# Optimization experiments

Hardware: AMD Instinct MI355X
Metric: run time of the kernel (lower is better)

Reference implementation:

```python
import jax, jax.numpy as jnp
import numpy as np

B, T, C, H = 2, 4096, 1024, 16
HD = C // H  # head dim = 64


def setup_inputs() -> dict:
    key = jax.random.key(0)
    ks = jax.random.split(key, 5)
    s = 1.0 / np.sqrt(C)
    return {
        "x": jax.random.normal(ks[0], (B, T, C), jnp.float32),
        # stored as (in, out) so forward is x @ w + b (equiv to torch Linear with W^T)
        "w_attn": jax.random.normal(ks[1], (C, 3 * C), jnp.float32) * s,
        "b_attn": jax.random.normal(ks[2], (3 * C,), jnp.float32) * 0.02,
        "w_proj": jax.random.normal(ks[3], (C, C), jnp.float32) * s,
        "b_proj": jax.random.normal(ks[4], (C,), jnp.float32) * 0.02,
    }


def reference(x, w_attn, b_attn, w_proj, b_proj):
    # qkv projection: (B,T,3C) -> split into q,k,v
    qkv = x @ w_attn + b_attn
    q, k, v = jnp.split(qkv, 3, axis=-1)
    # (B,T,C) -> (B,H,T,HD)
    def to_heads(t):
        return t.reshape(B, T, H, HD).transpose(0, 2, 1, 3)
    q, k, v = to_heads(q), to_heads(k), to_heads(v)
    # naive attention: explicit (B,H,T,T) scores, causal mask, softmax
    att = jnp.einsum("bhqd,bhkd->bhqk", q, k) * (1.0 / np.sqrt(HD))
    causal = jnp.tril(jnp.ones((T, T), bool))  # (T,T)
    att = jnp.where(causal[None, None], att, -jnp.inf)
    att = jax.nn.softmax(att, axis=-1)
    y = jnp.einsum("bhqk,bhkd->bhqd", att, v)  # (B,H,T,HD)
    y = y.transpose(0, 2, 1, 3).reshape(B, T, C)
    y = y @ w_proj + b_proj
    return (y, (k, v))
```

## Files before the change

kernel.cpp:

```cpp
#include <hip/hip_runtime.h>
#include <hip/hip_bf16.h>

typedef unsigned short u16;
typedef __attribute__((ext_vector_type(8))) short short8;
typedef __attribute__((ext_vector_type(4))) short s16x4;
typedef __attribute__((ext_vector_type(4))) float f32x4;

#define T_SEQ  4096
#define HEADS  16
#define HDIM   64
#define CDIM   1024
#define MDIM   8192
#define HSZ    (T_SEQ * HDIM)
#define SEC    8388608
#define QSCALE 0.1803368801111244f

__device__ __forceinline__ u16 f2bf(float f) {
    __hip_bfloat16 h = __float2bfloat16(f);
    u16 u; __builtin_memcpy(&u, &h, 2);
    return u;
}

__global__ __launch_bounds__(256) void cast_k(const float* __restrict__ in,
                                              u16* __restrict__ out, int n4) {
    const int i = blockIdx.x * 256 + threadIdx.x;
    if (i < n4) {
        f32x4 v = ((const f32x4*)in)[i];
        s16x4 o;
        #pragma unroll
        for (int j = 0; j < 4; ++j) o[j] = (short)f2bf(v[j]);
        ((s16x4*)out)[i] = o;
    }
}

template <int IN_F32, int PERM5>
__global__ __launch_bounds__(256) void transpose_k(const void* __restrict__ in_,
                                                   u16* __restrict__ out,
                                                   int R, int C) {
    __shared__ u16 tile[32][33];
    const size_t zoff = (size_t)blockIdx.z * R * C;
    const int c0 = blockIdx.x * 32, r0 = blockIdx.y * 32;
    const int tx = threadIdx.x, ty = threadIdx.y;
    #pragma unroll
    for (int i = ty; i < 32; i += 8) {
        const size_t idx = zoff + (size_t)(r0 + i) * C + c0 + tx;
        tile[i][tx] = IN_F32 ? f2bf(((const float*)in_)[idx])
                             : ((const u16*)in_)[idx];
    }
    __syncthreads();
    const int txo = PERM5 ? (((tx & 12) << 1) + (tx & 3) + ((tx & 16) >> 2)) : tx;
    #pragma unroll
    for (int i = ty; i < 32; i += 8)
        out[zoff + (size_t)(c0 + i) * R + r0 + txo] = tile[tx][i];
}

template <int MODE>
__global__ __launch_bounds__(256) void gemm_k(const u16* __restrict__ A,
                                              const u16* __restrict__ Bt,
                                              const float* __restrict__ bias,
                                              float* __restrict__ outp,
                                              u16* __restrict__ qws,
                                              u16* __restrict__ kbf, int K) {
    __shared__ unsigned char sA[16384];
    __shared__ unsigned char sB[16384];
    const int tid  = threadIdx.x;
    const int lane = tid & 63;
    const int w = tid >> 6, wr = w >> 1, wc = w & 1;
    const int m0 = blockIdx.y * 128, n0 = blockIdx.x * 128;
    const int fr = lane & 15, fg = lane >> 4;

    f32x4 acc[4][4] = {};

    const int lrow  = lane >> 3;
    const int gcole = ((lane & 7) ^ lrow) << 3;
    const u16* gaw = A  + (size_t)(m0 + w * 32 + lrow) * K + gcole;
    const u16* gbw = Bt + (size_t)(n0 + w * 32 + lrow) * K + gcole;
    const int rswz = (fr & 7) << 4;

    const int nk = K >> 6;
    for (int kt = 0; kt < nk; ++kt) {
        __syncthreads();
        #pragma unroll
        for (int i = 0; i < 4; ++i) {
            __builtin_amdgcn_global_load_lds(
                (const __attribute__((address_space(1))) void*)(gaw + (size_t)i * 8 * K),
                (__attribute__((address_space(3))) void*)(sA + w * 4096 + i * 1024),
                16, 0, 0);
            __builtin_amdgcn_global_load_lds(
                (const __attribute__((address_space(1))) void*)(gbw + (size_t)i * 8 * K),
                (__attribute__((address_space(3))) void*)(sB + w * 4096 + i * 1024),
                16, 0, 0);
        }
        gaw += 64; gbw += 64;
        __syncthreads();

        #pragma unroll
        for (int kk = 0; kk < 2; ++kk) {
            short8 af[4], bf[4];
            #pragma unroll
            for (int m = 0; m < 4; ++m)
                af[m] = *(const short8*)(sA + (wr*64 + m*16 + fr) * 128 +
                                         ((kk*64 + fg*16) ^ rswz));
            #pragma unroll
            for (int n = 0; n < 4; ++n)
                bf[n] = *(const short8*)(sB + (wc*64 + n*16 + fr) * 128 +
                                         ((kk*64 + fg*16) ^ rswz));
            #pragma unroll
            for (int m = 0; m < 4; ++m)
                #pragma unroll
                for (int n = 0; n < 4; ++n)
                    acc[m][n] = __builtin_amdgcn_mfma_f32_16x16x32_bf16(
                        af[m], bf[n], acc[m][n], 0, 0, 0);
        }
    }

    #pragma unroll
    for (int n = 0; n < 4; ++n) {
        const int gn = n0 + wc*64 + n*16 + fr;
        const float bn = bias[gn];
        if (MODE == 0) {
            const int s = gn >> 10;
            const int c = gn & 1023;
            const int h = c >> 6, d = c & 63;
            if (s == 0) {
                #pragma unroll
                for (int m = 0; m < 4; ++m)
                    #pragma unroll
                    for (int r = 0; r < 4; ++r) {
                        const int gm = m0 + wr*64 + m*16 + fg*4 + r;
                        const int b = gm >> 12, t = gm & 4095;
                        qws[(size_t)((b << 4) + h) * HSZ + (size_t)t * HDIM + d] =
                            f2bf((acc[m][n][r] + bn) * QSCALE);
                    }
            } else {
                float* fdst = outp + (size_t)s * SEC;
                #pragma unroll
                for (int m = 0; m < 4; ++m)
                    #pragma unroll
                    for (int r = 0; r < 4; ++r) {
                        const int gm = m0 + wr*64 + m*16 + fg*4 + r;
                        const int b = gm >> 12, t = gm & 4095;
                        const size_t hidx =
                            (size_t)((b << 4) + h) * HSZ + (size_t)t * HDIM + d;
                        const float v = acc[m][n][r] + bn;
                        fdst[hidx] = v;
                        if (s == 1 && kbf) kbf[hidx] = f2bf(v);
                    }
            }
        } else {
            #pragma unroll
            for (int m = 0; m < 4; ++m)
                #pragma unroll
                for (int r = 0; r < 4; ++r) {
                    const int gm = m0 + wr*64 + m*16 + fg*4 + r;
                    outp[(size_t)gm * CDIM + gn] = acc[m][n][r] + bn;
                }
        }
    }
}

template <int KBF>
__global__ __launch_bounds__(256) void attn_k(const u16* __restrict__ q,
                                              const float* __restrict__ kf32,
                                              const u16* __restrict__ kb16,
                                              const u16* __restrict__ vt,
                                              u16* __restrict__ att) {
    __shared__ unsigned char sK[8192];
    __shared__ unsigned char sV[8192];
    const int wg  = blockIdx.x;
    const int xcd = wg & 7;
    const int i   = wg >> 3;
    const int bh  = xcd * 4 + (i >> 5);
    const int pair = i & 31;
    const int tid = threadIdx.x, lane = tid & 63, w = tid >> 6;
    const int fr = lane & 15, fg = lane >> 4;
    const size_t hbase = (size_t)bh * HSZ;

    const int srow  = tid >> 2;
    const int scolb = (tid & 3) * 32;
    const int swz   = (srow & 7) << 4;
    const int rswz  = (fr & 7) << 4;

    const float* gkf = kf32 ? kf32 + hbase + (size_t)srow * 64 + (tid & 3) * 16 : nullptr;
    const u16*   gkb = kb16 ? kb16 + hbase + (size_t)srow * 64 + (tid & 3) * 16 : nullptr;
    const u16*   gv  = vt + hbase + (size_t)srow * T_SEQ + (tid & 3) * 16;
    unsigned char* sKw = sK + srow * 128;
    unsigned char* sVw = sV + srow * 128;
    const int b = bh >> 4, h = bh & 15;

    short8 ones;
    #pragma unroll
    for (int j = 0; j < 8; ++j) ones[j] = (short)0x3F80;

    #pragma unroll
    for (int ph = 0; ph < 2; ++ph) {
        const int qblk = ph ? 63 - pair : pair;
        const int q0 = qblk * 64 + w * 16;

        const short8 qf0 = *(const short8*)(q + hbase + (size_t)(q0 + fr) * 64 + fg * 8);
        const short8 qf1 = *(const short8*)(q + hbase + (size_t)(q0 + fr) * 64 + 32 + fg * 8);

        f32x4 o[4] = {};
        f32x4 o4 = {};

        const int n64 = qblk + 1;
        for (int k64 = 0; k64 < n64; ++k64) {
            short8 kv0, kv1;
            if (KBF) {
                kv0 = *(const short8*)(gkb + (size_t)k64 * 4096);
                kv1 = *(const short8*)(gkb + (size_t)k64 * 4096 + 8);
            } else {
                f32x4 a0 = *(const f32x4*)(gkf + (size_t)k64 * 4096);
                f32x4 a1 = *(const f32x4*)(gkf + (size_t)k64 * 4096 + 4);
                f32x4 a2 = *(const f32x4*)(gkf + (size_t)k64 * 4096 + 8);
                f32x4 a3 = *(const f32x4*)(gkf + (size_t)k64 * 4096 + 12);
                #pragma unroll
                for (int j = 0; j < 4; ++j) {
                    kv0[j]     = (short)f2bf(a0[j]);
                    kv0[4 + j] = (short)f2bf(a1[j]);
                    kv1[j]     = (short)f2bf(a2[j]);
                    kv1[4 + j] = (short)f2bf(a3[j]);
                }
            }
            short8 vv0 = *(const short8*)(gv + k64 * 64);
            short8 vv1 = *(const short8*)(gv + k64 * 64 + 8);
            __syncthreads();
            *(short8*)(sKw + ((scolb)      ^ swz)) = kv0;
            *(short8*)(sKw + ((scolb + 16) ^ swz)) = kv1;
            *(short8*)(sVw + ((scolb)      ^ swz)) = vv0;
            *(short8*)(sVw + ((scolb + 16) ^ swz)) = vv1;
            __syncthreads();

            #pragma unroll
            for (int tt = 0; tt < 2; ++tt) {
                const int kb2 = k64 * 64 + tt * 32;

                f32x4 z[2];
                #pragma unroll
                for (int kh = 0; kh < 2; ++kh) {
                    const unsigned char* Kr = sK + (tt*32 + kh*16 + fr) * 128;
                    short8 kfa = *(const short8*)(Kr + ((fg*16) ^ rswz));
                    short8 kfb = *(const short8*)(Kr + ((64 + fg*16) ^ rswz));
                    f32x4 zz = {0.f, 0.f, 0.f, 0.f};
                    zz = __builtin_amdgcn_mfma_f32_16x16x32_bf16(kfa, qf0, zz, 0, 0, 0);
                    zz = __builtin_amdgcn_mfma_f32_16x16x32_bf16(kfb, qf1, zz, 0, 0, 0);
                    z[kh] = zz;
                }

                const bool full = (kb2 + 31 <= q0);
                const int kq = kb2 + fg * 4;
                const int qg = q0 + fr;
                float p[8];
                #pragma unroll
                for (int r = 0; r < 4; ++r) {
                    float s0 = z[0][r], s1 = z[1][r];
                    if (!full) {
                        s0 = (kq + r      <= qg) ? s0 : -1e30f;
                        s1 = (kq + 16 + r <= qg) ? s1 : -1e30f;
                    }
                    p[r]     = exp2f(s0);
                    p[4 + r] = exp2f(s1);
                }

                unsigned int pw0, pw1, pw2, pw3;
                asm("v_cvt_pk_bf16_f32 %0, %1, %2" : "=v"(pw0) : "v"(p[0]), "v"(p[1]));
                asm("v_cvt_pk_bf16_f32 %0, %1, %2" : "=v"(pw1) : "v"(p[2]), "v"(p[3]));
                asm("v_cvt_pk_bf16_f32 %0, %1, %2" : "=v"(pw2) : "v"(p[4]), "v"(p[5]));
                asm("v_cvt_pk_bf16_f32 %0, %1, %2" : "=v"(pw3) : "v"(p[6]), "v"(p[7]));
                short8 pf;
                {
                    unsigned int tmp[4] = {pw0, pw1, pw2, pw3};
                    __builtin_memcpy(&pf, tmp, 16);
                }

                #pragma unroll
                for (int db = 0; db < 4; ++db) {
                    const unsigned char* Vr = sV + (db*16 + fr) * 128;
                    short8 vf = *(const short8*)(Vr + ((tt*64 + fg*16) ^ rswz));
                    o[db] = __builtin_amdgcn_mfma_f32_16x16x32_bf16(pf, vf, o[db], 0, 0, 0);
                }
                o4 = __builtin_amdgcn_mfma_f32_16x16x32_bf16(pf, ones, o4, 0, 0, 0);
            }
        }

        #pragma unroll
        for (int r = 0; r < 4; ++r) {
            const float invq = 1.f / o4[r];
            const int t = q0 + fg * 4 + r;
            #pragma unroll
            for (int db = 0; db < 4; ++db) {
                att[(size_t)(b * T_SEQ + t) * CDIM + h * 64 + db * 16 + fr] =
                    f2bf(o[db][r] * invq);
            }
        }
    }
}

extern "C" void kernel_launch(void* const* d_in, const int* in_sizes, int n_in,
                              void* d_out, int out_size, void* d_ws, size_t ws_size,
                              hipStream_t stream) {
    (void)out_size;
    const float *x = nullptr, *w_attn = nullptr, *b_attn = nullptr,
                *w_proj = nullptr, *b_proj = nullptr;
    for (int i = 0; i < n_in; ++i) {
        switch (in_sizes[i]) {
            case 8388608: x      = (const float*)d_in[i]; break;
            case 3145728: w_attn = (const float*)d_in[i]; break;
            case 3072:    b_attn = (const float*)d_in[i]; break;
            case 1048576: w_proj = (const float*)d_in[i]; break;
            case 1024:    b_proj = (const float*)d_in[i]; break;
        }
    }
    if (!x || !w_attn || !b_attn || !w_proj || !b_proj) return;

    float* out = (float*)d_out;
    unsigned char* ws = (unsigned char*)d_ws;
    const bool big = ws_size >= (64ull << 20);

    u16* q_ws = (u16*)(ws);
    u16* wTp  = (u16*)(ws);
    u16* x_bf = (u16*)(ws + 16777216);
    u16* vT   = (u16*)(ws + 16777216);
    u16* wTa  = (u16*)(ws + 33554432);
    u16* attb = (u16*)(ws + 33554432);
    u16* k_bf = big ? (u16*)(ws + 50331648) : nullptr;

    cast_k<<<8192, 256, 0, stream>>>(x, x_bf, 2097152);
    transpose_k<1, 0><<<dim3(96, 32, 1), dim3(32, 8), 0, stream>>>(w_attn, wTa, 1024, 3072);
    gemm_k<0><<<dim3(24, 64), 256, 0, stream>>>(x_bf, wTa, b_attn, out, q_ws, k_bf, 1024);
    transpose_k<1, 1><<<dim3(2, 128, 32), dim3(32, 8), 0, stream>>>(out + 2 * (size_t)SEC, vT, 4096, 64);
    if (big)
        attn_k<1><<<1024, 256, 0, stream>>>(q_ws, nullptr, k_bf, vT, attb);
    else
        attn_k<0><<<1024, 256, 0, stream>>>(q_ws, out + SEC, nullptr, vT, attb);
    transpose_k<1, 0><<<dim3(32, 32, 1), dim3(32, 8), 0, stream>>>(w_proj, wTp, 1024, 1024);
    gemm_k<1><<<dim3(8, 64), 256, 0, stream>>>(attb, wTp, b_proj, out, nullptr, nullptr, 1024);
}
```

Before: 261.8 us.

## Share K/V tile loads between paired low and high query blocks in attention

The attention kernel used to handle its two query blocks (pair and 63-pair) one after the other, reloading the same K/V tiles for the low block's range. It now walks the shared key range once and computes both query blocks against each staged K/V tile, then finishes the high block's remaining tiles on its own. This removes roughly a third of the global K/V loads, LDS stores and barriers per workgroup, and skips the mask check for the high block in the shared range. In exchange each thread keeps two sets of accumulators and Q fragments live, which raises register pressure.

```diff
diff --git a/kernel.cpp b/kernel.cpp
--- a/kernel.cpp
+++ b/kernel.cpp
@@ -159,6 +159,59 @@
     }
 }
 
+template <int ALWAYS_FULL>
+__device__ __forceinline__ void attn_sub(
+    const unsigned char* sK, const unsigned char* sV,
+    short8 qf0, short8 qf1, short8 ones, int q0, int kb2, int tt,
+    f32x4 (&o)[4], f32x4& o4, int fr, int fg, int rswz)
+{
+    f32x4 z[2];
+    #pragma unroll
+    for (int kh = 0; kh < 2; ++kh) {
+        const unsigned char* Kr = sK + (tt*32 + kh*16 + fr) * 128;
+        short8 kfa = *(const short8*)(Kr + ((fg*16) ^ rswz));
+        short8 kfb = *(const short8*)(Kr + ((64 + fg*16) ^ rswz));
+        f32x4 zz = {0.f, 0.f, 0.f, 0.f};
+        zz = __builtin_amdgcn_mfma_f32_16x16x32_bf16(kfa, qf0, zz, 0, 0, 0);
+        zz = __builtin_amdgcn_mfma_f32_16x16x32_bf16(kfb, qf1, zz, 0, 0, 0);
+        z[kh] = zz;
+    }
+
+    const bool full = ALWAYS_FULL || (kb2 + 31 <= q0);
+    const int kq = kb2 + fg * 4;
+    const int qg = q0 + fr;
+    float p[8];
+    #pragma unroll
+    for (int r = 0; r < 4; ++r) {
+        float s0 = z[0][r], s1 = z[1][r];
+        if (!full) {
+            s0 = (kq + r      <= qg) ? s0 : -1e30f;
+            s1 = (kq + 16 + r <= qg) ? s1 : -1e30f;
+        }
+        p[r]     = exp2f(s0);
+        p[4 + r] = exp2f(s1);
+    }
+
+    unsigned int pw0, pw1, pw2, pw3;
+    asm("v_cvt_pk_bf16_f32 %0, %1, %2" : "=v"(pw0) : "v"(p[0]), "v"(p[1]));
+    asm("v_cvt_pk_bf16_f32 %0, %1, %2" : "=v"(pw1) : "v"(p[2]), "v"(p[3]));
+    asm("v_cvt_pk_bf16_f32 %0, %1, %2" : "=v"(pw2) : "v"(p[4]), "v"(p[5]));
+    asm("v_cvt_pk_bf16_f32 %0, %1, %2" : "=v"(pw3) : "v"(p[6]), "v"(p[7]));
+    short8 pf;
+    {
+        unsigned int tmp[4] = {pw0, pw1, pw2, pw3};
+        __builtin_memcpy(&pf, tmp, 16);
+    }
+
+    #pragma unroll
+    for (int db = 0; db < 4; ++db) {
+        const unsigned char* Vr = sV + (db*16 + fr) * 128;
+        short8 vf = *(const short8*)(Vr + ((tt*64 + fg*16) ^ rswz));
+        o[db] = __builtin_amdgcn_mfma_f32_16x16x32_bf16(pf, vf, o[db], 0, 0, 0);
+    }
+    o4 = __builtin_amdgcn_mfma_f32_16x16x32_bf16(pf, ones, o4, 0, 0, 0);
+}
+
 template <int KBF>
 __global__ __launch_bounds__(256) void attn_k(const u16* __restrict__ q,
                                               const float* __restrict__ kf32,
@@ -192,106 +245,106 @@
     #pragma unroll
     for (int j = 0; j < 8; ++j) ones[j] = (short)0x3F80;
 
-    #pragma unroll
-    for (int ph = 0; ph < 2; ++ph) {
-        const int qblk = ph ? 63 - pair : pair;
-        const int q0 = qblk * 64 + w * 16;
-
-        const short8 qf0 = *(const short8*)(q + hbase + (size_t)(q0 + fr) * 64 + fg * 8);
-        const short8 qf1 = *(const short8*)(q + hbase + (size_t)(q0 + fr) * 64 + 32 + fg * 8);
-
-        f32x4 o[4] = {};
-        f32x4 o4 = {};
-
-        const int n64 = qblk + 1;
-        for (int k64 = 0; k64 < n64; ++k64) {
-            short8 kv0, kv1;
-            if (KBF) {
-                kv0 = *(const short8*)(gkb + (size_t)k64 * 4096);
-                kv1 = *(const short8*)(gkb + (size_t)k64 * 4096 + 8);
-            } else {
-                f32x4 a0 = *(const f32x4*)(gkf + (size_t)k64 * 4096);
-                f32x4 a1 = *(const f32x4*)(gkf + (size_t)k64 * 4096 + 4);
-                f32x4 a2 = *(const f32x4*)(gkf + (size_t)k64 * 4096 + 8);
-                f32x4 a3 = *(const f32x4*)(gkf + (size_t)k64 * 4096 + 12);
-                #pragma unroll
-                for (int j = 0; j < 4; ++j) {
-                    kv0[j]     = (short)f2bf(a0[j]);
-                    kv0[4 + j] = (short)f2bf(a1[j]);
-                    kv1[j]     = (short)f2bf(a2[j]);
-                    kv1[4 + j] = (short)f2bf(a3[j]);
-                }
+    const int qblkL = pair, qblkH = 63 - pair;
+    const int q0l = qblkL * 64 + w * 16;
+    const int q0h = qblkH * 64 + w * 16;
+
+    const short8 qf0l = *(const short8*)(q + hbase + (size_t)(q0l + fr) * 64 + fg * 8);
+    const short8 qf1l = *(const short8*)(q + hbase + (size_t)(q0l + fr) * 64 + 32 + fg * 8);
+    const short8 qf0h = *(const short8*)(q + hbase + (size_t)(q0h + fr) * 64 + fg * 8);
+    const short8 qf1h = *(const short8*)(q + hbase + (size_t)(q0h + fr) * 64 + 32 + fg * 8);
+
+    f32x4 oL[4] = {}, oH[4] = {};
+    f32x4 o4L = {}, o4H = {};
+
+    for (int k64 = 0; k64 <= pair; ++k64) {
+        short8 kv0, kv1;
+        if (KBF) {
+            kv0 = *(const short8*)(gkb + (size_t)k64 * 4096);
+            kv1 = *(const short8*)(gkb + (size_t)k64 * 4096 + 8);
+        } else {
+            f32x4 a0 = *(const f32x4*)(gkf + (size_t)k64 * 4096);
+            f32x4 a1 = *(const f32x4*)(gkf + (size_t)k64 * 4096 + 4);
+            f32x4 a2 = *(const f32x4*)(gkf + (size_t)k64 * 4096 + 8);
+            f32x4 a3 = *(const f32x4*)(gkf + (size_t)k64 * 4096 + 12);
+            #pragma unroll
+            for (int j = 0; j < 4; ++j) {
+                kv0[j]     = (short)f2bf(a0[j]);
+                kv0[4 + j] = (short)f2bf(a1[j]);
+                kv1[j]     = (short)f2bf(a2[j]);
+                kv1[4 + j] = (short)f2bf(a3[j]);
             }
-            short8 vv0 = *(const short8*)(gv + k64 * 64);
-            short8 vv1 = *(const short8*)(gv + k64 * 64 + 8);
-            __syncthreads();
-            *(short8*)(sKw + ((scolb)      ^ swz)) = kv0;
-            *(short8*)(sKw + ((scolb + 16) ^ swz)) = kv1;
-            *(short8*)(sVw + ((scolb)      ^ swz)) = vv0;
-            *(short8*)(sVw + ((scolb + 16) ^ swz)) = vv1;
-            __syncthreads();
-
-            #pragma unroll
-            for (int tt = 0; tt < 2; ++tt) {
-                const int kb2 = k64 * 64 + tt * 32;
-
-                f32x4 z[2];
-                #pragma unroll
-                for (int kh = 0; kh < 2; ++kh) {
-                    const unsigned char* Kr = sK + (tt*32 + kh*16 + fr) * 128;
-                    short8 kfa = *(const short8*)(Kr + ((fg*16) ^ rswz));
-                    short8 kfb = *(const short8*)(Kr + ((64 + fg*16) ^ rswz));
-                    f32x4 zz = {0.f, 0.f, 0.f, 0.f};
-                    zz = __builtin_amdgcn_mfma_f32_16x16x32_bf16(kfa, qf0, zz, 0, 0, 0);
-                    zz = __builtin_amdgcn_mfma_f32_16x16x32_bf16(kfb, qf1, zz, 0, 0, 0);
-                    z[kh] = zz;
-                }
-
-                const bool full = (kb2 + 31 <= q0);
-                const int kq = kb2 + fg * 4;
-                const int qg = q0 + fr;
-                float p[8];
-                #pragma unroll
-                for (int r = 0; r < 4; ++r) {
-                    float s0 = z[0][r], s1 = z[1][r];
-                    if (!full) {
-                        s0 = (kq + r      <= qg) ? s0 : -1e30f;
-                        s1 = (kq + 16 + r <= qg) ? s1 : -1e30f;
-                    }
-                    p[r]     = exp2f(s0);
-                    p[4 + r] = exp2f(s1);
-                }
-
-                unsigned int pw0, pw1, pw2, pw3;
-                asm("v_cvt_pk_bf16_f32 %0, %1, %2" : "=v"(pw0) : "v"(p[0]), "v"(p[1]));
-                asm("v_cvt_pk_bf16_f32 %0, %1, %2" : "=v"(pw1) : "v"(p[2]), "v"(p[3]));
-                asm("v_cvt_pk_bf16_f32 %0, %1, %2" : "=v"(pw2) : "v"(p[4]), "v"(p[5]));
-                asm("v_cvt_pk_bf16_f32 %0, %1, %2" : "=v"(pw3) : "v"(p[6]), "v"(p[7]));
-                short8 pf;
-                {
-                    unsigned int tmp[4] = {pw0, pw1, pw2, pw3};
-                    __builtin_memcpy(&pf, tmp, 16);
-                }
-
-                #pragma unroll
-                for (int db = 0; db < 4; ++db) {
-                    const unsigned char* Vr = sV + (db*16 + fr) * 128;
-                    short8 vf = *(const short8*)(Vr + ((tt*64 + fg*16) ^ rswz));
-                    o[db] = __builtin_amdgcn_mfma_f32_16x16x32_bf16(pf, vf, o[db], 0, 0, 0);
-                }
-                o4 = __builtin_amdgcn_mfma_f32_16x16x32_bf16(pf, ones, o4, 0, 0, 0);
+        }
+        short8 vv0 = *(const short8*)(gv + k64 * 64);
+        short8 vv1 = *(const short8*)(gv + k64 * 64 + 8);
+        __syncthreads();
+        *(short8*)(sKw + ((scolb)      ^ swz)) = kv0;
+        *(short8*)(sKw + ((scolb + 16) ^ swz)) = kv1;
+        *(short8*)(sVw + ((scolb)      ^ swz)) = vv0;
+        *(short8*)(sVw + ((scolb + 16) ^ swz)) = vv1;
+        __syncthreads();
+
+        #pragma unroll
+        for (int tt = 0; tt < 2; ++tt) {
+            const int kb2 = k64 * 64 + tt * 32;
+            attn_sub<1>(sK, sV, qf0h, qf1h, ones, q0h, kb2, tt, oH, o4H, fr, fg, rswz);
+            attn_sub<0>(sK, sV, qf0l, qf1l, ones, q0l, kb2, tt, oL, o4L, fr, fg, rswz);
+        }
+    }
+
+    #pragma unroll
+    for (int r = 0; r < 4; ++r) {
+        const float invq = 1.f / o4L[r];
+        const int t = q0l + fg * 4 + r;
+        #pragma unroll
+        for (int db = 0; db < 4; ++db) {
+            att[(size_t)(b * T_SEQ + t) * CDIM + h * 64 + db * 16 + fr] =
+                f2bf(oL[db][r] * invq);
+        }
+    }
+
+    for (int k64 = pair + 1; k64 <= qblkH; ++k64) {
+        short8 kv0, kv1;
+        if (KBF) {
+            kv0 = *(const short8*)(gkb + (size_t)k64 * 4096);
+            kv1 = *(const short8*)(gkb + (size_t)k64 * 4096 + 8);
+        } else {
+            f32x4 a0 = *(const f32x4*)(gkf + (size_t)k64 * 4096);
+            f32x4 a1 = *(const f32x4*)(gkf + (size_t)k64 * 4096 + 4);
+            f32x4 a2 = *(const f32x4*)(gkf + (size_t)k64 * 4096 + 8);
+            f32x4 a3 = *(const f32x4*)(gkf + (size_t)k64 * 4096 + 12);
+            #pragma unroll
+            for (int j = 0; j < 4; ++j) {
+                kv0[j]     = (short)f2bf(a0[j]);
+                kv0[4 + j] = (short)f2bf(a1[j]);
+                kv1[j]     = (short)f2bf(a2[j]);
+                kv1[4 + j] = (short)f2bf(a3[j]);
             }
         }
-
-        #pragma unroll
-        for (int r = 0; r < 4; ++r) {
-            const float invq = 1.f / o4[r];
-            const int t = q0 + fg * 4 + r;
-            #pragma unroll
-            for (int db = 0; db < 4; ++db) {
-                att[(size_t)(b * T_SEQ + t) * CDIM + h * 64 + db * 16 + fr] =
-                    f2bf(o[db][r] * invq);
-            }
+        short8 vv0 = *(const short8*)(gv + k64 * 64);
+        short8 vv1 = *(const short8*)(gv + k64 * 64 + 8);
+        __syncthreads();
+        *(short8*)(sKw + ((scolb)      ^ swz)) = kv0;
+        *(short8*)(sKw + ((scolb + 16) ^ swz)) = kv1;
+        *(short8*)(sVw + ((scolb)      ^ swz)) = vv0;
+        *(short8*)(sVw + ((scolb + 16) ^ swz)) = vv1;
+        __syncthreads();
+
+        #pragma unroll
+        for (int tt = 0; tt < 2; ++tt) {
+            const int kb2 = k64 * 64 + tt * 32;
+            attn_sub<0>(sK, sV, qf0h, qf1h, ones, q0h, kb2, tt, oH, o4H, fr, fg, rswz);
+        }
+    }
+
+    #pragma unroll
+    for (int r = 0; r < 4; ++r) {
+        const float invq = 1.f / o4H[r];
+        const int t = q0h + fg * 4 + r;
+        #pragma unroll
+        for (int db = 0; db < 4; ++db) {
+            att[(size_t)(b * T_SEQ + t) * CDIM + h * 64 + db * 16 + fr] =
+                f2bf(oH[db][r] * invq);
         }
     }
 }
```

Measured after the change: 264.4 us. About the same (+1.0%).
